# Performance work log

Hardware: AMD Instinct MI355X
Metric: run time of the kernel (lower is better)

Reference implementation:

```python
import jax, jax.numpy as jnp
import numpy as np


def setup_inputs() -> dict:
    key = jax.random.key(0)
    k1, k2, k3, k4, k5 = jax.random.split(key, 5)
    B, S, E2, D = 32, 2048, 1024, 512
    return {
        "output_encoder": jax.random.normal(k1, (B, S, E2), dtype=jnp.float32),
        "last_hidden_decoder": jax.random.normal(k2, (B, D), dtype=jnp.float32),
        "W_att": jax.random.normal(k3, (E2 + D, D), dtype=jnp.float32) * 0.02,
        "b_att": jax.random.normal(k4, (D,), dtype=jnp.float32) * 0.02,
        "v": jax.random.normal(k5, (D,), dtype=jnp.float32) * 0.02,
    }


def reference(output_encoder, last_hidden_decoder, W_att, b_att, v):
    # output_encoder: (B, S, E2); last_hidden_decoder: (B, D)
    B, S, E2 = output_encoder.shape
    D = last_hidden_decoder.shape[-1]
    # Split W_att to avoid materializing the repeated+concat tensor:
    # concat(enc, dec) @ W == enc @ W_enc + dec @ W_dec  (dec broadcast over seq)
    W_enc, W_dec = W_att[:E2], W_att[E2:]
    dec_proj = last_hidden_decoder @ W_dec  # (B, D)
    energy = jnp.tanh(jnp.einsum("bse,ed->bsd", output_encoder, W_enc)
                      + dec_proj[:, None, :] + b_att)  # (B, S, D)
    attention = jnp.einsum("bsd,d->bs", energy, v)  # (B, S)
    attention_weights = jax.nn.softmax(attention, axis=1)  # (B, S)
    # context: (B, 1, E2)
    context = jnp.einsum("bs,bse->be", attention_weights, output_encoder)[:, None, :]
    return context
```

## Files before the change

### kernel.cpp

```cpp
#include <hip/hip_runtime.h>
#include <stdint.h>


typedef __attribute__((ext_vector_type(8))) __bf16 bf16x8;
typedef __attribute__((ext_vector_type(4))) float f32x4;

__device__ __forceinline__ uint16_t f32_to_bf16_rne(float f) {
  union { float f; uint32_t u; } v; v.f = f;
  uint32_t u = v.u;
  return (uint16_t)((u + 0x7FFFu + ((u >> 16) & 1u)) >> 16);
}

__device__ __forceinline__ float tanh_fast(float x) {
  float e = __expf(2.0f * x);
  return 1.0f - 2.0f * __builtin_amdgcn_rcpf(e + 1.0f);
}

__global__ __launch_bounds__(256) void prep_kernel(
    const float* __restrict__ dec,
    const float* __restrict__ Watt,
    const float* __restrict__ batt,
    float* __restrict__ cbias,
    uint16_t* __restrict__ Wb,
    float* __restrict__ out)
{
  const int t = blockIdx.x * 256 + threadIdx.x;

  for (int i = t; i < 32768; i += 16384) out[i] = 0.0f;

  {
    const int b = t >> 9, d = t & 511;
    const float* wd = Watt + 1024 * 512 + d;
    const float* dv = dec + b * 512;
    float s0 = 0.f, s1 = 0.f, s2 = 0.f, s3 = 0.f;
    #pragma unroll 4
    for (int k = 0; k < 512; k += 4) {
      s0 += dv[k + 0] * wd[(k + 0) * 512];
      s1 += dv[k + 1] * wd[(k + 1) * 512];
      s2 += dv[k + 2] * wd[(k + 2) * 512];
      s3 += dv[k + 3] * wd[(k + 3) * 512];
    }
    cbias[t] = batt[d] + ((s0 + s1) + (s2 + s3));
  }

  uint4* WbV = (uint4*)Wb;
  #pragma unroll
  for (int i = 0; i < 4; ++i) {
    const int u = t + 16384 * i;
    const int c  = u >> 11;
    const int w  = u & 2047;
    const int d  = w >> 2;
    const int tt = w & 3;
    const int kb = c * 32 + ((tt ^ ((d >> 1) & 3)) << 3);
    uint32_t h[8];
    #pragma unroll
    for (int kk = 0; kk < 8; ++kk) {
      float f = Watt[(size_t)(kb + kk) * 512 + d];
      h[kk] = f32_to_bf16_rne(f);
    }
    uint4 val;
    val.x = h[0] | (h[1] << 16);
    val.y = h[2] | (h[3] << 16);
    val.z = h[4] | (h[5] << 16);
    val.w = h[6] | (h[7] << 16);
    WbV[u] = val;
  }
}

__global__ __launch_bounds__(512, 4) void energy_kernel(
    const float* __restrict__ x,
    const uint16_t* __restrict__ Wb,
    const float* __restrict__ cbias,
    const float* __restrict__ vvec,
    float* __restrict__ att)
{
  __shared__ __align__(16) uint8_t AL[2][64 * 64];
  __shared__ __align__(16) uint8_t BL[2][512 * 64];

  const int tid  = threadIdx.x;
  const int lane = tid & 63;
  const int wave = tid >> 6;
  const int l15  = lane & 15;
  const int l4   = lane >> 4;
  const int brow0 = blockIdx.x * 64;
  const int b     = brow0 >> 11;

  const int r_st = tid >> 3, q_st = tid & 7;
  const int aoff = r_st * 64 + ((q_st * 8) ^ (((r_st >> 1) & 3) << 4));
  const float* asrc = x + (size_t)(brow0 + r_st) * 1024 + q_st * 4;
  const uint8_t* wbase = (const uint8_t*)Wb + (lane << 4);

  f32x4 acc[4][4];
  #pragma unroll
  for (int mf = 0; mf < 4; ++mf)
    #pragma unroll
    for (int nf = 0; nf < 4; ++nf)
      acc[mf][nf] = (f32x4){0.f, 0.f, 0.f, 0.f};

  float4 av = *(const float4*)(asrc);
  #pragma unroll
  for (int i = 0; i < 4; ++i) {
    const int u = i * 8 + wave;
    __builtin_amdgcn_global_load_lds(
        (const __attribute__((address_space(1))) uint32_t*)(wbase + u * 1024),
        (__attribute__((address_space(3))) uint32_t*)(&BL[0][u * 1024]),
        16, 0, 0);
  }

  #pragma unroll 2
  for (int c = 0; c < 32; ++c) {
    uint8_t* Ab = AL[c & 1];
    uint8_t* Bb = BL[c & 1];

    {
      uint32_t lo = (uint32_t)f32_to_bf16_rne(av.x) | ((uint32_t)f32_to_bf16_rne(av.y) << 16);
      uint32_t hi = (uint32_t)f32_to_bf16_rne(av.z) | ((uint32_t)f32_to_bf16_rne(av.w) << 16);
      *(uint2*)(Ab + aoff) = make_uint2(lo, hi);
    }

    if (c < 31) {
      av = *(const float4*)(asrc + (c + 1) * 32);
      asm volatile("s_waitcnt vmcnt(1)" ::: "memory");
    } else {
      asm volatile("s_waitcnt vmcnt(0)" ::: "memory");
    }
    asm volatile("s_waitcnt lgkmcnt(0)" ::: "memory");
    __builtin_amdgcn_s_barrier();
    asm volatile("" ::: "memory");

    if (c < 31) {
      const uint8_t* wc = wbase + ((size_t)(c + 1) << 15);
      uint8_t* Bn = BL[(c + 1) & 1];
      #pragma unroll
      for (int i = 0; i < 4; ++i) {
        const int u = i * 8 + wave;
        __builtin_amdgcn_global_load_lds(
            (const __attribute__((address_space(1))) uint32_t*)(wc + u * 1024),
            (__attribute__((address_space(3))) uint32_t*)(Bn + u * 1024),
            16, 0, 0);
      }
    }

    bf16x8 af[4], bfr[4];
    #pragma unroll
    for (int mf = 0; mf < 4; ++mf) {
      const int r = mf * 16 + l15;
      af[mf] = *(const bf16x8*)(Ab + r * 64 + ((l4 * 16) ^ (((r >> 1) & 3) << 4)));
    }
    #pragma unroll
    for (int nf = 0; nf < 4; ++nf) {
      const int d = wave * 64 + nf * 16 + l15;
      bfr[nf] = *(const bf16x8*)(Bb + d * 64 + ((l4 * 16) ^ (((d >> 1) & 3) << 4)));
    }
    #pragma unroll
    for (int mf = 0; mf < 4; ++mf)
      #pragma unroll
      for (int nf = 0; nf < 4; ++nf)
        acc[mf][nf] = __builtin_amdgcn_mfma_f32_16x16x32_bf16(af[mf], bfr[nf], acc[mf][nf], 0, 0, 0);
  }

  float cb[4], vv[4];
  #pragma unroll
  for (int nf = 0; nf < 4; ++nf) {
    const int d = wave * 64 + nf * 16 + l15;
    cb[nf] = cbias[b * 512 + d];
    vv[nf] = vvec[d];
  }

  __syncthreads();
  float* red = (float*)AL;
  if (tid < 64) red[tid] = 0.0f;
  __syncthreads();

  #pragma unroll
  for (int mf = 0; mf < 4; ++mf) {
    float s[4] = {0.f, 0.f, 0.f, 0.f};
    #pragma unroll
    for (int nf = 0; nf < 4; ++nf) {
      #pragma unroll
      for (int j = 0; j < 4; ++j) {
        const float e = acc[mf][nf][j] + cb[nf];
        s[j] += tanh_fast(e) * vv[nf];
      }
    }
    #pragma unroll
    for (int j = 0; j < 4; ++j) {
      float r = s[j];
      r += __shfl_xor(r, 1);
      r += __shfl_xor(r, 2);
      r += __shfl_xor(r, 4);
      r += __shfl_xor(r, 8);
      if (l15 == 0) atomicAdd(&red[mf * 16 + 4 * l4 + j], r);
    }
  }
  __syncthreads();
  if (tid < 64) att[brow0 + tid] = red[tid];
}

__global__ __launch_bounds__(256) void softmax_kernel(float* __restrict__ att) {
  const int b = blockIdx.x;
  float* row = att + b * 2048;
  const int tid = threadIdx.x;
  __shared__ float redm[4], reds[4];

  float vals[8];
  float m = -1e30f;
  #pragma unroll
  for (int i = 0; i < 8; ++i) { vals[i] = row[tid + 256 * i]; m = fmaxf(m, vals[i]); }
  #pragma unroll
  for (int msk = 1; msk < 64; msk <<= 1) m = fmaxf(m, __shfl_xor(m, msk));
  if ((tid & 63) == 0) redm[tid >> 6] = m;
  __syncthreads();
  m = fmaxf(fmaxf(redm[0], redm[1]), fmaxf(redm[2], redm[3]));

  float s = 0.f;
  #pragma unroll
  for (int i = 0; i < 8; ++i) { vals[i] = __expf(vals[i] - m); s += vals[i]; }
  #pragma unroll
  for (int msk = 1; msk < 64; msk <<= 1) s += __shfl_xor(s, msk);
  if ((tid & 63) == 0) reds[tid >> 6] = s;
  __syncthreads();
  const float inv = 1.0f / (((reds[0] + reds[1]) + (reds[2] + reds[3])));
  #pragma unroll
  for (int i = 0; i < 8; ++i) row[tid + 256 * i] = vals[i] * inv;
}

__global__ __launch_bounds__(256) void context_kernel(
    const float* __restrict__ x,
    const float* __restrict__ w,
    float* __restrict__ out)
{
  const int blk = blockIdx.x;
  const int b = blk >> 4, sc = blk & 15;
  const int tid = threadIdx.x;
  const float* xb = x + ((size_t)(b * 2048 + sc * 128)) * 1024 + tid * 4;
  const float* wb = w + b * 2048 + sc * 128;

  float4 acc = {0.f, 0.f, 0.f, 0.f};
  for (int si = 0; si < 128; ++si) {
    const float ww = wb[si];
    const float4 xv = *(const float4*)(xb + (size_t)si * 1024);
    acc.x += ww * xv.x;
    acc.y += ww * xv.y;
    acc.z += ww * xv.z;
    acc.w += ww * xv.w;
  }
  float* o = out + b * 1024 + tid * 4;
  atomicAdd(o + 0, acc.x);
  atomicAdd(o + 1, acc.y);
  atomicAdd(o + 2, acc.z);
  atomicAdd(o + 3, acc.w);
}

extern "C" void kernel_launch(void* const* d_in, const int* in_sizes, int n_in,
                              void* d_out, int out_size, void* d_ws, size_t ws_size,
                              hipStream_t stream) {
  const float* x    = (const float*)d_in[0];
  const float* dec  = (const float*)d_in[1];
  const float* Watt = (const float*)d_in[2];
  const float* batt = (const float*)d_in[3];
  const float* v    = (const float*)d_in[4];
  float* out = (float*)d_out;

  uint8_t* ws = (uint8_t*)d_ws;
  float*    att   = (float*)ws;
  float*    cbias = (float*)(ws + 256 * 1024);
  uint16_t* Wb    = (uint16_t*)(ws + 320 * 1024);

  prep_kernel<<<64, 256, 0, stream>>>(dec, Watt, batt, cbias, Wb, out);
  energy_kernel<<<1024, 512, 0, stream>>>(x, Wb, cbias, v, att);
  softmax_kernel<<<32, 256, 0, stream>>>(att);
  context_kernel<<<512, 256, 0, stream>>>(x, att, out);
}
```

Before: 156.2 us.

## Load W fragments directly into registers in MFMA order, drop B LDS staging

The bf16 weight layout is rearranged in the prep kernel so each wave's 16-lane MFMA B fragments are contiguous, and the energy kernel now loads them straight from global/L2 into registers with a double-buffered register ping-pong. This removes the 64KB B LDS buffer and its global_load_lds traffic, cutting LDS footprint and reads. It relies on every block re-reading W through cache with no LDS sharing across waves, and on the per-chunk A barrier alone for ordering.

```diff
diff --git a/kernel.cpp b/kernel.cpp
--- a/kernel.cpp
+++ b/kernel.cpp
@@ -46,12 +46,14 @@
   uint4* WbV = (uint4*)Wb;
   #pragma unroll
   for (int i = 0; i < 4; ++i) {
-    const int u = t + 16384 * i;
-    const int c  = u >> 11;
-    const int w  = u & 2047;
-    const int d  = w >> 2;
-    const int tt = w & 3;
-    const int kb = c * 32 + ((tt ^ ((d >> 1) & 3)) << 3);
+    const int u   = t + 16384 * i;
+    const int c   = u >> 11;
+    const int rem = u & 2047;
+    const int wn  = rem >> 8;
+    const int nf  = (rem >> 6) & 3;
+    const int ln  = rem & 63;
+    const int kb  = c * 32 + ((ln >> 4) << 3);
+    const int d   = wn * 64 + nf * 16 + (ln & 15);
     uint32_t h[8];
     #pragma unroll
     for (int kk = 0; kk < 8; ++kk) {
@@ -75,7 +77,6 @@
     float* __restrict__ att)
 {
   __shared__ __align__(16) uint8_t AL[2][64 * 64];
-  __shared__ __align__(16) uint8_t BL[2][512 * 64];
 
   const int tid  = threadIdx.x;
   const int lane = tid & 63;
@@ -88,7 +89,7 @@
   const int r_st = tid >> 3, q_st = tid & 7;
   const int aoff = r_st * 64 + ((q_st * 8) ^ (((r_st >> 1) & 3) << 4));
   const float* asrc = x + (size_t)(brow0 + r_st) * 1024 + q_st * 4;
-  const uint8_t* wbase = (const uint8_t*)Wb + (lane << 4);
+  const uint8_t* wslice = (const uint8_t*)Wb + (size_t)wave * 4096 + (size_t)lane * 16;
 
   f32x4 acc[4][4];
   #pragma unroll
@@ -97,67 +98,49 @@
     for (int nf = 0; nf < 4; ++nf)
       acc[mf][nf] = (f32x4){0.f, 0.f, 0.f, 0.f};
 
-  float4 av = *(const float4*)(asrc);
-  #pragma unroll
-  for (int i = 0; i < 4; ++i) {
-    const int u = i * 8 + wave;
-    __builtin_amdgcn_global_load_lds(
-        (const __attribute__((address_space(1))) uint32_t*)(wbase + u * 1024),
-        (__attribute__((address_space(3))) uint32_t*)(&BL[0][u * 1024]),
-        16, 0, 0);
-  }
-
-  #pragma unroll 2
-  for (int c = 0; c < 32; ++c) {
-    uint8_t* Ab = AL[c & 1];
-    uint8_t* Bb = BL[c & 1];
-
-    {
-      uint32_t lo = (uint32_t)f32_to_bf16_rne(av.x) | ((uint32_t)f32_to_bf16_rne(av.y) << 16);
-      uint32_t hi = (uint32_t)f32_to_bf16_rne(av.z) | ((uint32_t)f32_to_bf16_rne(av.w) << 16);
-      *(uint2*)(Ab + aoff) = make_uint2(lo, hi);
-    }
-
-    if (c < 31) {
-      av = *(const float4*)(asrc + (c + 1) * 32);
-      asm volatile("s_waitcnt vmcnt(1)" ::: "memory");
-    } else {
-      asm volatile("s_waitcnt vmcnt(0)" ::: "memory");
-    }
-    asm volatile("s_waitcnt lgkmcnt(0)" ::: "memory");
-    __builtin_amdgcn_s_barrier();
-    asm volatile("" ::: "memory");
-
-    if (c < 31) {
-      const uint8_t* wc = wbase + ((size_t)(c + 1) << 15);
-      uint8_t* Bn = BL[(c + 1) & 1];
-      #pragma unroll
-      for (int i = 0; i < 4; ++i) {
-        const int u = i * 8 + wave;
-        __builtin_amdgcn_global_load_lds(
-            (const __attribute__((address_space(1))) uint32_t*)(wc + u * 1024),
-            (__attribute__((address_space(3))) uint32_t*)(Bn + u * 1024),
-            16, 0, 0);
-      }
-    }
-
-    bf16x8 af[4], bfr[4];
-    #pragma unroll
-    for (int mf = 0; mf < 4; ++mf) {
-      const int r = mf * 16 + l15;
-      af[mf] = *(const bf16x8*)(Ab + r * 64 + ((l4 * 16) ^ (((r >> 1) & 3) << 4)));
-    }
-    #pragma unroll
-    for (int nf = 0; nf < 4; ++nf) {
-      const int d = wave * 64 + nf * 16 + l15;
-      bfr[nf] = *(const bf16x8*)(Bb + d * 64 + ((l4 * 16) ^ (((d >> 1) & 3) << 4)));
-    }
-    #pragma unroll
-    for (int mf = 0; mf < 4; ++mf)
-      #pragma unroll
-      for (int nf = 0; nf < 4; ++nf)
-        acc[mf][nf] = __builtin_amdgcn_mfma_f32_16x16x32_bf16(af[mf], bfr[nf], acc[mf][nf], 0, 0, 0);
-  }
+  float4 av_cur = *(const float4*)(asrc);
+  bf16x8 bA[4], bB[4];
+  {
+    const bf16x8* bs = (const bf16x8*)(wslice);
+    bA[0] = bs[0]; bA[1] = bs[64]; bA[2] = bs[128]; bA[3] = bs[192];
+  }
+
+#define CHUNK(C, BCUR, BNXT)                                                   \
+  {                                                                            \
+    const int c_ = (C);                                                        \
+    uint8_t* Ab = AL[c_ & 1];                                                  \
+    uint32_t lo_ = (uint32_t)f32_to_bf16_rne(av_cur.x) |                       \
+                   ((uint32_t)f32_to_bf16_rne(av_cur.y) << 16);                \
+    uint32_t hi_ = (uint32_t)f32_to_bf16_rne(av_cur.z) |                       \
+                   ((uint32_t)f32_to_bf16_rne(av_cur.w) << 16);                \
+    *(uint2*)(Ab + aoff) = make_uint2(lo_, hi_);                               \
+    const int cn_ = (c_ < 31) ? c_ + 1 : 31;                                   \
+    av_cur = *(const float4*)(asrc + cn_ * 32);                                \
+    asm volatile("s_waitcnt lgkmcnt(0)" ::: "memory");                         \
+    __builtin_amdgcn_s_barrier();                                              \
+    asm volatile("" ::: "memory");                                             \
+    {                                                                          \
+      const bf16x8* bs_ = (const bf16x8*)(wslice + (size_t)cn_ * 32768);       \
+      BNXT[0] = bs_[0]; BNXT[1] = bs_[64];                                     \
+      BNXT[2] = bs_[128]; BNXT[3] = bs_[192];                                  \
+    }                                                                          \
+    _Pragma("unroll")                                                          \
+    for (int mf = 0; mf < 4; ++mf) {                                           \
+      const int r_ = mf * 16 + l15;                                            \
+      bf16x8 afm = *(const bf16x8*)(Ab + r_ * 64 +                             \
+                                    ((l4 * 16) ^ (((r_ >> 1) & 3) << 4)));     \
+      acc[mf][0] = __builtin_amdgcn_mfma_f32_16x16x32_bf16(afm, BCUR[0], acc[mf][0], 0, 0, 0); \
+      acc[mf][1] = __builtin_amdgcn_mfma_f32_16x16x32_bf16(afm, BCUR[1], acc[mf][1], 0, 0, 0); \
+      acc[mf][2] = __builtin_amdgcn_mfma_f32_16x16x32_bf16(afm, BCUR[2], acc[mf][2], 0, 0, 0); \
+      acc[mf][3] = __builtin_amdgcn_mfma_f32_16x16x32_bf16(afm, BCUR[3], acc[mf][3], 0, 0, 0); \
+    }                                                                          \
+  }
+
+  for (int c = 0; c < 32; c += 2) {
+    CHUNK(c, bA, bB);
+    CHUNK(c + 1, bB, bA);
+  }
+#undef CHUNK
 
   float cb[4], vv[4];
   #pragma unroll
```

Measured after the change: 143.8 us. -8.0%, faster.
